# Optimization experiments

Hardware: AMD Instinct MI355X
Metric: run time of the kernel (lower is better)

Reference implementation:

```python
import jax, jax.numpy as jnp
import numpy as np

ALIGNED_H, ALIGNED_W = 7, 7          # module init args
AH, AW = ALIGNED_H + 1, ALIGNED_W + 1  # RoIAlignFunction sampling grid (8x8)


def setup_inputs() -> dict:
    key = jax.random.key(0)
    k1, k2, k3, k4 = jax.random.split(key, 4)
    B, C, H, W = 4, 256, 200, 200
    N = 1024
    spatial_scale = jnp.float32(1.0 / 16.0)
    img = H / (1.0 / 16.0)  # 3200 px image-space extent
    features = jax.random.normal(k1, (B, C, H, W), dtype=jnp.float32)
    bidx = jax.random.randint(k2, (N,), 0, B).astype(jnp.float32)
    xy1 = jax.random.uniform(k3, (N, 2), minval=0.0, maxval=img - 64.0)
    wh = jax.random.uniform(k4, (N, 2), minval=16.0, maxval=512.0)
    xy2 = jnp.minimum(xy1 + wh, img - 1.0)
    rois = jnp.concatenate(
        [bidx[:, None], xy1[:, 0:1], xy1[:, 1:2], xy2[:, 0:1], xy2[:, 1:2]], axis=1
    ).astype(jnp.float32)
    return {"features": features, "rois": rois, "spatial_scale": spatial_scale}


def _roi_align(features, rois, spatial_scale):
    B, C, H, W = features.shape
    b = rois[:, 0].astype(jnp.int32)
    x1 = rois[:, 1] * spatial_scale
    y1 = rois[:, 2] * spatial_scale
    x2 = rois[:, 3] * spatial_scale
    y2 = rois[:, 4] * spatial_scale
    bin_h = jnp.maximum(y2 - y1 + 1.0, 0.0) / (AH - 1)   # [N]
    bin_w = jnp.maximum(x2 - x1 + 1.0, 0.0) / (AW - 1)
    ph = jnp.arange(AH, dtype=features.dtype)
    pw = jnp.arange(AW, dtype=features.dtype)
    h = y1[:, None] + ph * bin_h[:, None]                 # [N, AH] sample rows
    w = x1[:, None] + pw * bin_w[:, None]                 # [N, AW] sample cols
    hs_f = jnp.minimum(jnp.floor(h), H - 2.0)             # clip as in CUDA kernel
    ws_f = jnp.minimum(jnp.floor(w), W - 2.0)
    hr = h - hs_f                                         # bilinear ratios
    wr = w - ws_f
    hi = jnp.clip(hs_f, 0.0, None).astype(jnp.int32)      # safe gather indices
    wi = jnp.clip(ws_f, 0.0, None).astype(jnp.int32)
    valid = ((h >= 0) & (h < H))[:, :, None] & ((w >= 0) & (w < W))[:, None, :]
    bb = b[:, None, None]
    Hg = hi[:, :, None]
    Wg = wi[:, None, :]

    def g(dh, dw):
        # advanced-index gather -> [N, AH, AW, C]
        return features[bb, :, Hg + dh, Wg + dw]

    hr_ = hr[:, :, None, None]
    wr_ = wr[:, None, :, None]
    val = (g(0, 0) * (1 - hr_) * (1 - wr_)
           + g(0, 1) * (1 - hr_) * wr_
           + g(1, 0) * hr_ * (1 - wr_)
           + g(1, 1) * hr_ * wr_)
    val = jnp.where(valid[..., None], val, 0.0)
    return jnp.transpose(val, (0, 3, 1, 2))               # [N, C, AH, AW]


def reference(features, rois, spatial_scale):
    x = _roi_align(features, rois, spatial_scale)
    # avg_pool2d(kernel_size=2, stride=1): 8x8 -> 7x7
    return (x[:, :, :-1, :-1] + x[:, :, :-1, 1:]
            + x[:, :, 1:, :-1] + x[:, :, 1:, 1:]) * 0.25
```

## Files before the change

kernel.cpp:

```cpp
#include <hip/hip_runtime.h>

#define BATCH 4
#define CH    256
#define FH    200
#define FW    200
#define NROI  1024
#define PLANE (FH * FW)
#define POOL  7
#define NWAVE 16

__global__ __launch_bounds__(1024, 1) void roialign_lds_kernel(
    const float* __restrict__ feat,
    const float* __restrict__ rois,
    const float* __restrict__ scale_p,
    float* __restrict__ out)
{
    __shared__ float splane[PLANE];

    const int c   = blockIdx.x;
    const int b   = blockIdx.y;
    const int tid = threadIdx.x;

    {
        const float4* __restrict__ src =
            (const float4*)(feat + ((size_t)b * CH + c) * PLANE);
        float4* dst = (float4*)splane;
        for (int i = tid; i < PLANE / 4; i += 1024)
            dst[i] = src[i];
    }
    __syncthreads();

    const float scale = scale_p[0];
    const int wave = tid >> 6;
    const int lane = tid & 63;
    const int ph   = lane >> 3;
    const int pw   = lane & 7;
    const bool do_store = (ph < POOL) && (pw < POOL);

    for (int n = wave; n < NROI; n += NWAVE) {
        const int rb = (int)rois[n * 5 + 0];
        if (rb != b) continue;

        const float x1 = rois[n * 5 + 1] * scale;
        const float y1 = rois[n * 5 + 2] * scale;
        const float x2 = rois[n * 5 + 3] * scale;
        const float y2 = rois[n * 5 + 4] * scale;

        const float bin_h = fmaxf(y2 - y1 + 1.0f, 0.0f) * (1.0f / 7.0f);
        const float bin_w = fmaxf(x2 - x1 + 1.0f, 0.0f) * (1.0f / 7.0f);

        const float h    = y1 + (float)ph * bin_h;
        const float w    = x1 + (float)pw * bin_w;
        const float hs_f = fminf(floorf(h), (float)(FH - 2));
        const float ws_f = fminf(floorf(w), (float)(FW - 2));
        const float hr   = h - hs_f;
        const float wr   = w - ws_f;
        const int   hi   = (int)fmaxf(hs_f, 0.0f);
        const int   wi   = (int)fmaxf(ws_f, 0.0f);
        const bool  valid = (h >= 0.0f) && (h < (float)FH) &&
                            (w >= 0.0f) && (w < (float)FW);
        const float m = valid ? 0.25f : 0.0f;

        const float w00 = (1.0f - hr) * (1.0f - wr) * m;
        const float w01 = (1.0f - hr) * wr * m;
        const float w10 = hr * (1.0f - wr) * m;
        const float w11 = hr * wr * m;

        const int off = hi * FW + wi;
        const float g00 = splane[off];
        const float g01 = splane[off + 1];
        const float g10 = splane[off + FW];
        const float g11 = splane[off + FW + 1];

        float v  = g00 * w00 + g01 * w01 + g10 * w10 + g11 * w11;

        float s1 = v + __shfl_down(v, 1, 64);
        float s2 = s1 + __shfl_down(s1, 8, 64);

        if (do_store)
            __builtin_nontemporal_store(
                s2, out + ((size_t)n * CH + c) * (POOL * POOL) + ph * POOL + pw);
    }
}

extern "C" void kernel_launch(void* const* d_in, const int* in_sizes, int n_in,
                              void* d_out, int out_size, void* d_ws, size_t ws_size,
                              hipStream_t stream) {
    const float* feat    = (const float*)d_in[0];
    const float* rois    = (const float*)d_in[1];
    const float* scale_p = (const float*)d_in[2];
    float*       out     = (float*)d_out;
    (void)in_sizes; (void)n_in; (void)out_size; (void)d_ws; (void)ws_size;

    dim3 grid(CH, BATCH);
    dim3 block(1024);
    hipLaunchKernelGGL(roialign_lds_kernel, grid, block, 0, stream,
                       feat, rois, scale_p, out);
}
```

Baseline: 320.0 us.

## Bucket RoIs per batch in a prepass so LDS kernel skips other batches

New measurement: 273.1 us. 14.7% less time.

```diff
diff --git a/kernel.cpp b/kernel.cpp
--- a/kernel.cpp
+++ b/kernel.cpp
@@ -9,10 +9,26 @@
 #define POOL  7
 #define NWAVE 16
 
+__global__ __launch_bounds__(1024) void build_roi_lists(
+    const float* __restrict__ rois, int* __restrict__ cnt, int* __restrict__ idx)
+{
+    __shared__ int lcnt[BATCH];
+    const int tid = threadIdx.x;
+    if (tid < BATCH) lcnt[tid] = 0;
+    __syncthreads();
+    const int b = (int)rois[tid * 5];
+    const int pos = atomicAdd(&lcnt[b], 1);
+    idx[(b << 10) + pos] = tid;
+    __syncthreads();
+    if (tid < BATCH) cnt[tid] = lcnt[tid];
+}
+
 __global__ __launch_bounds__(1024, 1) void roialign_lds_kernel(
     const float* __restrict__ feat,
     const float* __restrict__ rois,
     const float* __restrict__ scale_p,
+    const int*   __restrict__ cnt,
+    const int*   __restrict__ idx,
     float* __restrict__ out)
 {
     __shared__ float splane[PLANE];
@@ -37,9 +53,12 @@
     const int pw   = lane & 7;
     const bool do_store = (ph < POOL) && (pw < POOL);
 
-    for (int n = wave; n < NROI; n += NWAVE) {
-        const int rb = (int)rois[n * 5 + 0];
-        if (rb != b) continue;
+    const int cntb = __builtin_amdgcn_readfirstlane(cnt[b]);
+
+#pragma unroll 2
+    for (int i = wave; i < cntb; i += NWAVE) {
+        int n = idx[(b << 10) + i];
+        n = __builtin_amdgcn_readfirstlane(n);
 
         const float x1 = rois[n * 5 + 1] * scale;
         const float y1 = rois[n * 5 + 2] * scale;
@@ -83,6 +102,44 @@
     }
 }
 
+#define CGROUPS 8
+#define CH_PER_WAVE 8
+__global__ __launch_bounds__(256) void roialign_gather_kernel(
+    const float* __restrict__ feat, const float* __restrict__ rois,
+    const float* __restrict__ scale_p, float* __restrict__ out)
+{
+    const int n = blockIdx.x, g = blockIdx.y, tid = threadIdx.x;
+    const int wave = tid >> 6, lane = tid & 63;
+    const int ph = lane >> 3, pw = lane & 7;
+    const float scale = scale_p[0];
+    const int   b  = (int)rois[n * 5 + 0];
+    const float x1 = rois[n * 5 + 1] * scale, y1 = rois[n * 5 + 2] * scale;
+    const float x2 = rois[n * 5 + 3] * scale, y2 = rois[n * 5 + 4] * scale;
+    const float bin_h = fmaxf(y2 - y1 + 1.0f, 0.0f) / 7.0f;
+    const float bin_w = fmaxf(x2 - x1 + 1.0f, 0.0f) / 7.0f;
+    const float h = y1 + (float)ph * bin_h, w = x1 + (float)pw * bin_w;
+    const float hs_f = fminf(floorf(h), (float)(FH - 2));
+    const float ws_f = fminf(floorf(w), (float)(FW - 2));
+    const float hr = h - hs_f, wr = w - ws_f;
+    const int hi = (int)fmaxf(hs_f, 0.0f), wi = (int)fmaxf(ws_f, 0.0f);
+    const bool valid = (h >= 0.0f) && (h < (float)FH) && (w >= 0.0f) && (w < (float)FW);
+    const float m = valid ? 0.25f : 0.0f;
+    const float w00 = (1.0f - hr) * (1.0f - wr) * m, w01 = (1.0f - hr) * wr * m;
+    const float w10 = hr * (1.0f - wr) * m, w11 = hr * wr * m;
+    const int c0 = g * (4 * CH_PER_WAVE) + wave * CH_PER_WAVE;
+    const float* p = feat + ((size_t)(b * CH + c0)) * PLANE + (size_t)(hi * FW + wi);
+    float* outp = out + ((size_t)n * CH + c0) * (POOL * POOL) + ph * POOL + pw;
+    const bool do_store = (ph < POOL) && (pw < POOL);
+#pragma unroll
+    for (int dc = 0; dc < CH_PER_WAVE; ++dc) {
+        float v = p[0] * w00 + p[1] * w01 + p[FW] * w10 + p[FW + 1] * w11;
+        float s1 = v + __shfl_down(v, 1, 64);
+        float s2 = s1 + __shfl_down(s1, 8, 64);
+        if (do_store) __builtin_nontemporal_store(s2, outp);
+        p += PLANE; outp += POOL * POOL;
+    }
+}
+
 extern "C" void kernel_launch(void* const* d_in, const int* in_sizes, int n_in,
                               void* d_out, int out_size, void* d_ws, size_t ws_size,
                               hipStream_t stream) {
@@ -90,10 +147,18 @@
     const float* rois    = (const float*)d_in[1];
     const float* scale_p = (const float*)d_in[2];
     float*       out     = (float*)d_out;
-    (void)in_sizes; (void)n_in; (void)out_size; (void)d_ws; (void)ws_size;
+    (void)in_sizes; (void)n_in; (void)out_size;
 
-    dim3 grid(CH, BATCH);
-    dim3 block(1024);
-    hipLaunchKernelGGL(roialign_lds_kernel, grid, block, 0, stream,
-                       feat, rois, scale_p, out);
+    const size_t ws_needed = (size_t)(BATCH + BATCH * NROI) * sizeof(int);
+    if (ws_size >= ws_needed) {
+        int* cnt = (int*)d_ws;
+        int* idx = cnt + BATCH;
+        hipLaunchKernelGGL(build_roi_lists, dim3(1), dim3(1024), 0, stream,
+                           rois, cnt, idx);
+        hipLaunchKernelGGL(roialign_lds_kernel, dim3(CH, BATCH), dim3(1024), 0,
+                           stream, feat, rois, scale_p, cnt, idx, out);
+    } else {
+        hipLaunchKernelGGL(roialign_gather_kernel, dim3(NROI, CGROUPS), dim3(256),
+                           0, stream, feat, rois, scale_p, out);
+    }
 }
```
